# Kernel tuning notes

Measured on AMD Instinct MI355X. Metric: run time of the kernel, lower is better.

Reference implementation:

```python
import jax, jax.numpy as jnp
import numpy as np

D_MODEL = 1024
N_HEADS = 16
HEAD_DIM = D_MODEL // N_HEADS
D_FF = 4096
EPS = 1e-5


def setup_inputs() -> dict:
    key = jax.random.key(0)
    ks = jax.random.split(key, 12)
    s = 0.02
    return {
        "x": jax.random.normal(ks[0], (2, 2048, D_MODEL), jnp.float32),
        "wq": jax.random.normal(ks[1], (D_MODEL, D_MODEL), jnp.float32) * s,
        "bq": jnp.zeros((D_MODEL,), jnp.float32),
        "wk": jax.random.normal(ks[2], (D_MODEL, D_MODEL), jnp.float32) * s,
        "bk": jnp.zeros((D_MODEL,), jnp.float32),
        "wv": jax.random.normal(ks[3], (D_MODEL, D_MODEL), jnp.float32) * s,
        "bv": jnp.zeros((D_MODEL,), jnp.float32),
        "wo": jax.random.normal(ks[4], (D_MODEL, D_MODEL), jnp.float32) * s,
        "bo": jnp.zeros((D_MODEL,), jnp.float32),
        "w1": jax.random.normal(ks[5], (D_MODEL, D_FF), jnp.float32) * s,
        "b1": jnp.zeros((D_FF,), jnp.float32),
        "w2": jax.random.normal(ks[6], (D_FF, D_MODEL), jnp.float32) * s,
        "b2": jnp.zeros((D_MODEL,), jnp.float32),
        "g1": jnp.ones((D_MODEL,), jnp.float32),
        "be1": jnp.zeros((D_MODEL,), jnp.float32),
        "g2": jnp.ones((D_MODEL,), jnp.float32),
        "be2": jnp.zeros((D_MODEL,), jnp.float32),
    }


def _layer_norm(x, g, b):
    mu = jnp.mean(x, axis=-1, keepdims=True)
    var = jnp.var(x, axis=-1, keepdims=True)
    return (x - mu) * jax.lax.rsqrt(var + EPS) * g + b


def reference(x, wq, bq, wk, bk, wv, bv, wo, bo, w1, b1, w2, b2, g1, be1, g2, be2):
    B, S, D = x.shape
    nx = _layer_norm(x, g1, be1)
    # projections -> [B, H, S, d]
    def split_heads(t):
        return t.reshape(B, S, N_HEADS, HEAD_DIM).transpose(0, 2, 1, 3)
    q = split_heads(nx @ wq + bq)
    k = split_heads(nx @ wk + bk)
    v = split_heads(nx @ wv + bv)
    scores = jnp.einsum("bhqd,bhkd->bhqk", q, k) / jnp.sqrt(jnp.float32(HEAD_DIM))
    attn = jax.nn.softmax(scores, axis=-1)
    out = jnp.einsum("bhqk,bhkd->bhqd", attn, v)
    out = out.transpose(0, 2, 1, 3).reshape(B, S, D)
    x = x + (out @ wo + bo)
    nx = _layer_norm(x, g2, be2)
    ff = jax.nn.relu(nx @ w1 + b1) @ w2 + b2
    return x + ff
```

## Files before the change

### kernel.cpp

```cpp
#include <hip/hip_runtime.h>


typedef __attribute__((ext_vector_type(8))) unsigned short u16x8;
typedef __attribute__((ext_vector_type(4))) unsigned short u16x4;
typedef __attribute__((ext_vector_type(8))) __bf16 bf16x8;
typedef __attribute__((ext_vector_type(4))) float f32x4;
typedef __attribute__((ext_vector_type(4))) unsigned int u32x4;

#define C_SCALE 0.1803368801111f

static __device__ __forceinline__ unsigned short f2b(float f) {
    return __builtin_bit_cast(unsigned short, (__bf16)f);
}
static __device__ __forceinline__ float b2f(unsigned short h) {
    unsigned u = ((unsigned)h) << 16;
    float f;
    __builtin_memcpy(&f, &u, 4);
    return f;
}

static __device__ __forceinline__ void async_cp16(
    const unsigned short* g, unsigned short* l)
{
    __builtin_amdgcn_global_load_lds(
        (const __attribute__((address_space(1))) unsigned int*)g,
        (__attribute__((address_space(3))) unsigned int*)l,
        16, 0, 0);
}

__global__ __launch_bounds__(256) void transpose_all_k(
    const float* __restrict__ wq, const float* __restrict__ wk,
    const float* __restrict__ wv, const float* __restrict__ wo,
    const float* __restrict__ w1, const float* __restrict__ w2,
    unsigned short* __restrict__ wqkvT, unsigned short* __restrict__ woT,
    unsigned short* __restrict__ w1T, unsigned short* __restrict__ w2T)
{
    __shared__ unsigned short tile[32][33];
    const int ti = blockIdx.x;
    const float* in;
    unsigned short* out;
    int R, C, bi, bj;
    float sc = 1.0f;
    if (ti < 4096) {
        R = 1024; C = 1024;
        bi = (ti & 1023) >> 5; bj = ti & 31;
        int z = ti >> 10;
        in = (z == 0) ? wq : (z == 1) ? wk : (z == 2) ? wv : wo;
        out = (z < 3) ? wqkvT + (size_t)z * 1024 * 1024 : woT;
        if (z == 1) sc = C_SCALE;
    } else if (ti < 8192) {
        R = 1024; C = 4096;
        int l = ti - 4096;
        bi = l >> 7; bj = l & 127;
        in = w1; out = w1T;
    } else {
        R = 4096; C = 1024;
        int l = ti - 8192;
        bi = l >> 5; bj = l & 31;
        in = w2; out = w2T;
    }
    const int tx = threadIdx.x & 31, ty = threadIdx.x >> 5;
#pragma unroll
    for (int rr = 0; rr < 4; ++rr) {
        int r = ty + rr * 8;
        tile[r][tx] = f2b(in[(size_t)(bi * 32 + r) * C + bj * 32 + tx] * sc);
    }
    __syncthreads();
#pragma unroll
    for (int rr = 0; rr < 4; ++rr) {
        int r = ty + rr * 8;
        out[(size_t)(bj * 32 + r) * R + bi * 32 + tx] = tile[tx][r];
    }
}

__global__ __launch_bounds__(256) void concat3_k(
    const float* __restrict__ a, const float* __restrict__ b,
    const float* __restrict__ c, float* __restrict__ o)
{
    int t = blockIdx.x * 256 + threadIdx.x;
    float v = (t < 1024) ? a[t]
            : ((t < 2048) ? b[t - 1024] * C_SCALE : c[t - 2048]);
    o[t] = v;
}

__global__ __launch_bounds__(256) void ln_kernel(
    const float* __restrict__ x, const float* __restrict__ g,
    const float* __restrict__ be, unsigned short* __restrict__ o)
{
    const int row = blockIdx.x;
    const int t = threadIdx.x;
    const float* xr = x + (size_t)row * 1024;
    float4 v4 = *reinterpret_cast<const float4*>(&xr[t * 4]);
    float f[4] = {v4.x, v4.y, v4.z, v4.w};
    float s = f[0] + f[1] + f[2] + f[3];
    float ss = f[0] * f[0] + f[1] * f[1] + f[2] * f[2] + f[3] * f[3];
#pragma unroll
    for (int d = 1; d < 64; d <<= 1) {
        s += __shfl_xor(s, d);
        ss += __shfl_xor(ss, d);
    }
    __shared__ float sb[4], ssb[4];
    const int wave = t >> 6;
    if ((t & 63) == 0) { sb[wave] = s; ssb[wave] = ss; }
    __syncthreads();
    s = sb[0] + sb[1] + sb[2] + sb[3];
    ss = ssb[0] + ssb[1] + ssb[2] + ssb[3];
    const float mu = s * (1.0f / 1024.0f);
    const float var = ss * (1.0f / 1024.0f) - mu * mu;
    const float rs = rsqrtf(var + 1e-5f);
    u16x4 r4;
#pragma unroll
    for (int j = 0; j < 4; ++j)
        r4[j] = f2b((f[j] - mu) * rs * g[t * 4 + j] + be[t * 4 + j]);
    *reinterpret_cast<u16x4*>(&o[(size_t)row * 1024 + t * 4]) = r4;
}

__global__ __launch_bounds__(256) void reduce_ln_kernel(
    const unsigned short* __restrict__ pa, const unsigned short* __restrict__ pb,
    const float* __restrict__ bias, const float* __restrict__ x,
    const float* __restrict__ g, const float* __restrict__ be,
    float* __restrict__ x2, unsigned short* __restrict__ o)
{
    const int row = blockIdx.x;
    const int t = threadIdx.x;
    const size_t base = (size_t)row * 1024 + t * 4;
    float4 x4 = *reinterpret_cast<const float4*>(&x[base]);
    float4 bb = *reinterpret_cast<const float4*>(&bias[t * 4]);
    float f[4] = {x4.x + bb.x, x4.y + bb.y, x4.z + bb.z, x4.w + bb.w};
#pragma unroll
    for (int z = 0; z < 2; ++z) {
        u16x4 va = *reinterpret_cast<const u16x4*>(&pa[(size_t)z * 4096 * 1024 + base]);
        u16x4 vb = *reinterpret_cast<const u16x4*>(&pb[(size_t)z * 4096 * 1024 + base]);
#pragma unroll
        for (int j = 0; j < 4; ++j) f[j] += b2f(va[j]) + b2f(vb[j]);
    }
    *reinterpret_cast<float4*>(&x2[base]) = {f[0], f[1], f[2], f[3]};
    float s = f[0] + f[1] + f[2] + f[3];
    float ss = f[0] * f[0] + f[1] * f[1] + f[2] * f[2] + f[3] * f[3];
#pragma unroll
    for (int d = 1; d < 64; d <<= 1) {
        s += __shfl_xor(s, d);
        ss += __shfl_xor(ss, d);
    }
    __shared__ float sb[4], ssb[4];
    const int wave = t >> 6;
    if ((t & 63) == 0) { sb[wave] = s; ssb[wave] = ss; }
    __syncthreads();
    s = sb[0] + sb[1] + sb[2] + sb[3];
    ss = ssb[0] + ssb[1] + ssb[2] + ssb[3];
    const float mu = s * (1.0f / 1024.0f);
    const float var = ss * (1.0f / 1024.0f) - mu * mu;
    const float rs = rsqrtf(var + 1e-5f);
    u16x4 r4;
#pragma unroll
    for (int j = 0; j < 4; ++j)
        r4[j] = f2b((f[j] - mu) * rs * g[t * 4 + j] + be[t * 4 + j]);
    *reinterpret_cast<u16x4*>(&o[base]) = r4;
}

__global__ __launch_bounds__(256) void reduce_out4_k(
    const unsigned short* __restrict__ pa, const unsigned short* __restrict__ pb,
    const float* __restrict__ bias, const float* __restrict__ x2,
    float* __restrict__ out)
{
    const size_t i4 = ((size_t)blockIdx.x * 256 + threadIdx.x) * 4;
    float4 x4 = *reinterpret_cast<const float4*>(&x2[i4]);
    float4 bb = *reinterpret_cast<const float4*>(&bias[i4 & 1023]);
    float a0 = x4.x + bb.x, a1 = x4.y + bb.y, a2 = x4.z + bb.z, a3 = x4.w + bb.w;
#pragma unroll
    for (int z = 0; z < 2; ++z) {
        u16x4 va = *reinterpret_cast<const u16x4*>(&pa[(size_t)z * 4096 * 1024 + i4]);
        u16x4 vb = *reinterpret_cast<const u16x4*>(&pb[(size_t)z * 4096 * 1024 + i4]);
        a0 += b2f(va[0]) + b2f(vb[0]);
        a1 += b2f(va[1]) + b2f(vb[1]);
        a2 += b2f(va[2]) + b2f(vb[2]);
        a3 += b2f(va[3]) + b2f(vb[3]);
    }
    *reinterpret_cast<float4*>(&out[i4]) = {a0, a1, a2, a3};
}

template<int MODE, int RELU>
__global__ __launch_bounds__(512, 1) void gemm256(
    const unsigned short* __restrict__ A, int lda,
    const unsigned short* __restrict__ Bt, int ldb,
    const float* __restrict__ bias,
    void* __restrict__ Cv, void* __restrict__ Cv2, int N, int Kloop)
{
    __shared__ unsigned short lds[3 * 16384];
    const int t = threadIdx.x;
    const int wave = t >> 6, lane = t & 63;
    const int quad = lane >> 4, l16 = lane & 15;
    const int wm = wave >> 2, wn = wave & 3;
    const int m0 = blockIdx.y * 256;
    const int n0 = blockIdx.x * 256;
    const int k0 = blockIdx.z * Kloop;
    const int NT = Kloop >> 5;

    const int sc_row = t >> 2;
    const int sc_cb  = (t & 3) ^ ((t >> 3) & 3);
    const unsigned short* Asrc = &A[(size_t)(m0 + sc_row) * lda + k0 + sc_cb * 8];
    const unsigned short* Bsrc = &Bt[(size_t)(n0 + sc_row) * ldb + k0 + sc_cb * 8];
    const size_t Astep = (size_t)128 * lda;
    const size_t Bstep = (size_t)128 * ldb;
    unsigned short* dstA = &lds[t * 8];
    unsigned short* dstB = &lds[8192 + t * 8];

    const int cb = quad ^ ((l16 >> 1) & 3);
    const int aoff = (wm * 128 + l16) * 32 + cb * 8;
    const int boff = 8192 + (wn * 64 + l16) * 32 + cb * 8;

    f32x4 acc[8][4];
#pragma unroll
    for (int mi = 0; mi < 8; ++mi)
#pragma unroll
        for (int ni = 0; ni < 4; ++ni) acc[mi][ni] = {0.f, 0.f, 0.f, 0.f};

    async_cp16(Asrc, dstA);
    async_cp16(Asrc + Astep, dstA + 4096);
    async_cp16(Bsrc, dstB);
    async_cp16(Bsrc + Bstep, dstB + 4096);
    if (NT > 1) {
        async_cp16(Asrc + 32, dstA + 16384);
        async_cp16(Asrc + Astep + 32, dstA + 16384 + 4096);
        async_cp16(Bsrc + 32, dstB + 16384);
        async_cp16(Bsrc + Bstep + 32, dstB + 16384 + 4096);
        asm volatile("s_waitcnt vmcnt(4)\n\ts_barrier" ::: "memory");
    } else {
        asm volatile("s_waitcnt vmcnt(0)\n\ts_barrier" ::: "memory");
    }

    for (int tt = 0; tt < NT; ++tt) {
        const int b = tt - (tt / 3) * 3;
        const unsigned short* Lb = &lds[b * 16384];
        const int pf = tt + 2;
        const int bp = (pf < NT) ? (pf - (pf / 3) * 3) * 16384 : 0;
        bf16x8 af[8], bfr[4];
        if (pf < NT) {
            async_cp16(Asrc + (size_t)pf * 32, &lds[bp] + t * 8);
            async_cp16(Asrc + Astep + (size_t)pf * 32, &lds[bp] + t * 8 + 4096);
        }
#pragma unroll
        for (int mi = 0; mi < 8; ++mi)
            af[mi] = __builtin_bit_cast(bf16x8,
                *reinterpret_cast<const u16x8*>(&Lb[aoff + mi * 512]));
        bfr[0] = __builtin_bit_cast(bf16x8,
            *reinterpret_cast<const u16x8*>(&Lb[boff]));
        bfr[1] = __builtin_bit_cast(bf16x8,
            *reinterpret_cast<const u16x8*>(&Lb[boff + 512]));
        __builtin_amdgcn_s_setprio(1);
#pragma unroll
        for (int mi = 0; mi < 8; ++mi) {
            acc[mi][0] = __builtin_amdgcn_mfma_f32_16x16x32_bf16(
                af[mi], bfr[0], acc[mi][0], 0, 0, 0);
            acc[mi][1] = __builtin_amdgcn_mfma_f32_16x16x32_bf16(
                af[mi], bfr[1], acc[mi][1], 0, 0, 0);
        }
        __builtin_amdgcn_s_setprio(0);
        if (pf < NT) {
            async_cp16(Bsrc + (size_t)pf * 32, &lds[bp + 8192] + t * 8);
            async_cp16(Bsrc + Bstep + (size_t)pf * 32, &lds[bp + 8192] + t * 8 + 4096);
        }
        bfr[2] = __builtin_bit_cast(bf16x8,
            *reinterpret_cast<const u16x8*>(&Lb[boff + 1024]));
        bfr[3] = __builtin_bit_cast(bf16x8,
            *reinterpret_cast<const u16x8*>(&Lb[boff + 1536]));
        __builtin_amdgcn_s_setprio(1);
#pragma unroll
        for (int mi = 0; mi < 8; ++mi) {
            acc[mi][2] = __builtin_amdgcn_mfma_f32_16x16x32_bf16(
                af[mi], bfr[2], acc[mi][2], 0, 0, 0);
            acc[mi][3] = __builtin_amdgcn_mfma_f32_16x16x32_bf16(
                af[mi], bfr[3], acc[mi][3], 0, 0, 0);
        }
        __builtin_amdgcn_s_setprio(0);
        if (tt + 1 < NT) {
            if (pf < NT)
                asm volatile("s_waitcnt vmcnt(4)\n\ts_barrier" ::: "memory");
            else
                asm volatile("s_waitcnt vmcnt(0)\n\ts_barrier" ::: "memory");
        }
    }

#pragma unroll
    for (int mi = 0; mi < 8; ++mi) {
        const int gr0 = m0 + wm * 128 + mi * 16 + quad * 4;
#pragma unroll
        for (int ni = 0; ni < 4; ++ni) {
            const int gc = n0 + wn * 64 + ni * 16 + l16;
            if (MODE == 2) {
                const float bv = bias[gc];
                if (gc < 2048) {
#pragma unroll
                    for (int r = 0; r < 4; ++r)
                        ((unsigned short*)Cv)[(size_t)(gr0 + r) * 2048 + gc] =
                            f2b(acc[mi][ni][r] + bv);
                } else {
                    u16x4 pk;
#pragma unroll
                    for (int r = 0; r < 4; ++r) pk[r] = f2b(acc[mi][ni][r] + bv);
                    const int bb = gr0 >> 11, s0 = gr0 & 2047;
                    *reinterpret_cast<u16x4*>(
                        &((unsigned short*)Cv2)[((size_t)bb * 1024 + (gc - 2048)) * 2048 + s0]) = pk;
                }
            } else if (MODE == 5) {
                unsigned short* base = (blockIdx.z < 2)
                    ? (unsigned short*)Cv  + (size_t)blockIdx.z * 4096 * N
                    : (unsigned short*)Cv2 + (size_t)(blockIdx.z - 2) * 4096 * N;
#pragma unroll
                for (int r = 0; r < 4; ++r)
                    base[(size_t)(gr0 + r) * N + gc] = f2b(acc[mi][ni][r]);
            } else {
                const float bv = bias[gc];
#pragma unroll
                for (int r = 0; r < 4; ++r) {
                    float v = acc[mi][ni][r] + bv;
                    if (RELU) v = fmaxf(v, 0.f);
                    ((unsigned short*)Cv)[(size_t)(gr0 + r) * N + gc] = f2b(v);
                }
            }
        }
    }
}

__global__ __launch_bounds__(256, 2) void attn_kernel(
    const unsigned short* __restrict__ qkb, const unsigned short* __restrict__ vbT,
    unsigned short* __restrict__ ao)
{
    __shared__ unsigned short lds[3 * 8192];
    const int t = threadIdx.x;
    const int lane = t & 63;
    const int quad = lane >> 4, l16 = lane & 15;
    const int wave = t >> 6;
    const int bh = blockIdx.y;
    const int b = bh >> 4, h = bh & 15;
    const int q0 = blockIdx.x * 128 + wave * 32;
    const size_t qk_base = (size_t)b * 2048 * 2048;
    const size_t vt_base = (size_t)b * 1024 * 2048 + (size_t)h * 64 * 2048;

    bf16x8 qf[2][2];
#pragma unroll
    for (int m = 0; m < 2; ++m)
#pragma unroll
        for (int kk = 0; kk < 2; ++kk)
            qf[m][kk] = __builtin_bit_cast(bf16x8, *reinterpret_cast<const u16x8*>(
                &qkb[qk_base + (size_t)(q0 + m * 16 + l16) * 2048 + h * 64 + kk * 32 + quad * 8]));

    u16x8 ones_u;
#pragma unroll
    for (int j = 0; j < 8; ++j) ones_u[j] = 0x3F80;
    const bf16x8 onesf = __builtin_bit_cast(bf16x8, ones_u);

    f32x4 o_acc[2][4], l_frag[2];
#pragma unroll
    for (int m = 0; m < 2; ++m) {
        l_frag[m] = {0.f, 0.f, 0.f, 0.f};
#pragma unroll
        for (int nf = 0; nf < 4; ++nf) o_acc[m][nf] = {0.f, 0.f, 0.f, 0.f};
    }

    const int c0 = t, c1 = t + 256;
    const int r0 = c0 >> 3, r1 = c1 >> 3;
    const int scb0 = (c0 & 7) ^ (r0 & 7), scb1 = (c1 & 7) ^ (r1 & 7);
    const unsigned short* kS0 = &qkb[qk_base + (size_t)r0 * 2048 + 1024 + h * 64 + scb0 * 8];
    const unsigned short* kS1 = &qkb[qk_base + (size_t)r1 * 2048 + 1024 + h * 64 + scb1 * 8];
    const unsigned short* vS0 = &vbT[vt_base + (size_t)r0 * 2048 + scb0 * 8];
    const unsigned short* vS1 = &vbT[vt_base + (size_t)r1 * 2048 + scb1 * 8];

    const int off0 = l16 * 64 + ((quad ^ (l16 & 7)) * 8);

#define STAGE(tile, buf)                                                      \
    {                                                                         \
        const size_t ko = (size_t)(tile) * 64 * 2048;                         \
        const int vo = (tile) * 64;                                           \
        async_cp16(kS0 + ko, &lds[(buf) * 8192 + c0 * 8]);                    \
        async_cp16(kS1 + ko, &lds[(buf) * 8192 + c1 * 8]);                    \
        async_cp16(vS0 + vo, &lds[(buf) * 8192 + 4096 + c0 * 8]);             \
        async_cp16(vS1 + vo, &lds[(buf) * 8192 + 4096 + c1 * 8]);             \
    }

    STAGE(0, 0);
    STAGE(1, 1);
    asm volatile("s_waitcnt vmcnt(4)\n\ts_barrier" ::: "memory");

    for (int tt = 0; tt < 32; ++tt) {
        const int buf = tt - (tt / 3) * 3;
        const int pf = tt + 2;
        if (pf < 32) {
            const int bp = pf - (pf / 3) * 3;
            STAGE(pf, bp);
        }
        const unsigned short* LK = &lds[buf * 8192];
        const unsigned short* LV = LK + 4096;

        unsigned d0[2][4], d1[2][4];
#pragma unroll
        for (int kf = 0; kf < 4; ++kf) {
            bf16x8 kfr0 = __builtin_bit_cast(bf16x8,
                *reinterpret_cast<const u16x8*>(&LK[off0 + kf * 1024]));
            bf16x8 kfr1 = __builtin_bit_cast(bf16x8,
                *reinterpret_cast<const u16x8*>(&LK[(off0 ^ 32) + kf * 1024]));
#pragma unroll
            for (int m = 0; m < 2; ++m) {
                f32x4 s = {0.f, 0.f, 0.f, 0.f};
                s = __builtin_amdgcn_mfma_f32_16x16x32_bf16(kfr0, qf[m][0], s, 0, 0, 0);
                s = __builtin_amdgcn_mfma_f32_16x16x32_bf16(kfr1, qf[m][1], s, 0, 0, 0);
                d0[m][kf] = (unsigned)f2b(exp2f(s[0])) |
                            ((unsigned)f2b(exp2f(s[1])) << 16);
                d1[m][kf] = (unsigned)f2b(exp2f(s[2])) |
                            ((unsigned)f2b(exp2f(s[3])) << 16);
            }
        }
#pragma unroll
        for (int kh = 0; kh < 2; ++kh) {
            bf16x8 pfr[2];
#pragma unroll
            for (int m = 0; m < 2; ++m) {
                unsigned x0 = d0[m][kh * 2], y0 = d0[m][kh * 2 + 1];
                unsigned x1 = d1[m][kh * 2], y1 = d1[m][kh * 2 + 1];
                asm("v_permlane32_swap_b32 %0, %1\n\t"
                    "v_permlane16_swap_b32 %0, %1"
                    : "+v"(x0), "+v"(y0));
                asm("v_permlane32_swap_b32 %0, %1\n\t"
                    "v_permlane16_swap_b32 %0, %1"
                    : "+v"(x1), "+v"(y1));
                u32x4 pw = {x0, x1, y0, y1};
                pfr[m] = __builtin_bit_cast(bf16x8, pw);
                l_frag[m] = __builtin_amdgcn_mfma_f32_16x16x32_bf16(
                    pfr[m], onesf, l_frag[m], 0, 0, 0);
            }
            __builtin_amdgcn_s_setprio(1);
#pragma unroll
            for (int nf = 0; nf < 4; ++nf) {
                bf16x8 vfr = __builtin_bit_cast(bf16x8,
                    *reinterpret_cast<const u16x8*>(&LV[(off0 ^ (kh * 32)) + nf * 1024]));
#pragma unroll
                for (int m = 0; m < 2; ++m)
                    o_acc[m][nf] = __builtin_amdgcn_mfma_f32_16x16x32_bf16(
                        pfr[m], vfr, o_acc[m][nf], 0, 0, 0);
            }
            __builtin_amdgcn_s_setprio(0);
        }
        if (tt + 1 < 32) {
            if (pf < 32)
                asm volatile("s_waitcnt vmcnt(4)\n\ts_barrier" ::: "memory");
            else
                asm volatile("s_waitcnt vmcnt(0)\n\ts_barrier" ::: "memory");
        }
    }
#undef STAGE

#pragma unroll
    for (int m = 0; m < 2; ++m) {
#pragma unroll
        for (int r = 0; r < 4; ++r) {
            const float inv = 1.0f / l_frag[m][r];
            const int row = q0 + m * 16 + quad * 4 + r;
#pragma unroll
            for (int nf = 0; nf < 4; ++nf)
                ao[(size_t)b * 2048 * 1024 + (size_t)row * 1024 + h * 64 + nf * 16 + l16] =
                    f2b(o_acc[m][nf][r] * inv);
        }
    }
}

extern "C" void kernel_launch(void* const* d_in, const int* in_sizes, int n_in,
                              void* d_out, int out_size, void* d_ws, size_t ws_size,
                              hipStream_t stream)
{
    const float* x   = (const float*)d_in[0];
    const float* wq  = (const float*)d_in[1];
    const float* bq  = (const float*)d_in[2];
    const float* wk  = (const float*)d_in[3];
    const float* bk  = (const float*)d_in[4];
    const float* wv  = (const float*)d_in[5];
    const float* bv  = (const float*)d_in[6];
    const float* wo  = (const float*)d_in[7];
    const float* bo  = (const float*)d_in[8];
    const float* w1  = (const float*)d_in[9];
    const float* b1  = (const float*)d_in[10];
    const float* w2  = (const float*)d_in[11];
    const float* b2  = (const float*)d_in[12];
    const float* g1  = (const float*)d_in[13];
    const float* be1 = (const float*)d_in[14];
    const float* g2  = (const float*)d_in[15];
    const float* be2 = (const float*)d_in[16];
    float* out = (float*)d_out;
    char*  ws  = (char*)d_ws;

    const int M = 4096, D = 1024, DFF = 4096;
    const size_t MB = 1 << 20;

    unsigned short* wqkvT = (unsigned short*)(ws + 0 * MB);
    unsigned short* woT   = (unsigned short*)(ws + 6 * MB);
    unsigned short* w1T   = (unsigned short*)(ws + 8 * MB);
    unsigned short* w2T   = (unsigned short*)(ws + 16 * MB);
    unsigned short* ln    = (unsigned short*)(ws + 24 * MB);
    unsigned short* qkb   = (unsigned short*)(ws + 32 * MB);
    unsigned short* vbT   = (unsigned short*)(ws + 48 * MB);
    unsigned short* ao    = (unsigned short*)(ws + 56 * MB);
    unsigned short* ff1   = (unsigned short*)(ws + 32 * MB);
    float*          x2    = (float*)(ws + 64 * MB);
    float*          bqkv  = (float*)(ws + 80 * MB);
    unsigned short* pHi   = (unsigned short*)(ws + 80 * MB);
    unsigned short* pOlo  = (unsigned short*)(ws + 32 * MB);
    unsigned short* pFlo  = (unsigned short*)(ws + 0 * MB);

    transpose_all_k<<<12288, 256, 0, stream>>>(wq, wk, wv, wo, w1, w2,
                                               wqkvT, woT, w1T, w2T);
    concat3_k<<<12, 256, 0, stream>>>(bq, bk, bv, bqkv);
    ln_kernel<<<M, 256, 0, stream>>>(x, g1, be1, ln);
    gemm256<2, 0><<<dim3(12, 16), 512, 0, stream>>>(
        ln, D, wqkvT, D, bqkv, qkb, vbT, 3072, D);
    attn_kernel<<<dim3(16, 32), 256, 0, stream>>>(qkb, vbT, ao);
    gemm256<5, 0><<<dim3(4, 16, 4), 512, 0, stream>>>(
        ao, D, woT, D, nullptr, pHi, pOlo, 1024, 256);
    reduce_ln_kernel<<<M, 256, 0, stream>>>(pHi, pOlo, bo, x, g2, be2, x2, ln);
    gemm256<0, 1><<<dim3(16, 16), 512, 0, stream>>>(
        ln, D, w1T, D, b1, ff1, nullptr, DFF, D);
    gemm256<5, 0><<<dim3(4, 16, 4), 512, 0, stream>>>(
        ff1, DFF, w2T, DFF, nullptr, pHi, pFlo, 1024, 1024);
    reduce_out4_k<<<4096, 256, 0, stream>>>(pHi, pFlo, b2, x2, out);
}
```

Baseline: 354.1 us.

## Switch GEMM to double-buffered BK=64 stages with 8-chunk XOR swizzle

The 256x256 GEMM kernel moves from a triple-buffered pipeline with 32-wide K slices to a double-buffered pipeline with 64-wide K slices, using 128 KB of LDS. The LDS layout and XOR swizzle change to 8 chunks per row, and each iteration runs two 32-wide MFMA half-steps. The aim is to halve the number of barriers and loop iterations and to issue larger batches of async copies. The cost is a shallower prefetch, since each step now waits for vmcnt(0) rather than keeping a stage in flight, which can expose global memory latency.

```diff
diff --git a/kernel.cpp b/kernel.cpp
--- a/kernel.cpp
+++ b/kernel.cpp
@@ -186,7 +186,7 @@
     const float* __restrict__ bias,
     void* __restrict__ Cv, void* __restrict__ Cv2, int N, int Kloop)
 {
-    __shared__ unsigned short lds[3 * 16384];
+    __shared__ unsigned short lds[65536];
     const int t = threadIdx.x;
     const int wave = t >> 6, lane = t & 63;
     const int quad = lane >> 4, l16 = lane & 15;
@@ -194,20 +194,35 @@
     const int m0 = blockIdx.y * 256;
     const int n0 = blockIdx.x * 256;
     const int k0 = blockIdx.z * Kloop;
-    const int NT = Kloop >> 5;
-
-    const int sc_row = t >> 2;
-    const int sc_cb  = (t & 3) ^ ((t >> 3) & 3);
-    const unsigned short* Asrc = &A[(size_t)(m0 + sc_row) * lda + k0 + sc_cb * 8];
-    const unsigned short* Bsrc = &Bt[(size_t)(n0 + sc_row) * ldb + k0 + sc_cb * 8];
-    const size_t Astep = (size_t)128 * lda;
-    const size_t Bstep = (size_t)128 * ldb;
-    unsigned short* dstA = &lds[t * 8];
-    unsigned short* dstB = &lds[8192 + t * 8];
-
-    const int cb = quad ^ ((l16 >> 1) & 3);
-    const int aoff = (wm * 128 + l16) * 32 + cb * 8;
-    const int boff = 8192 + (wn * 64 + l16) * 32 + cb * 8;
+    const int NT = Kloop >> 6;
+
+    const unsigned short* Ap[4];
+    const unsigned short* Bp[4];
+#pragma unroll
+    for (int j = 0; j < 4; ++j) {
+        const int c = t + j * 512;
+        const int row = c >> 3;
+        const int gcb = (c & 7) ^ (row & 7);
+        Ap[j] = &A[(size_t)(m0 + row) * lda + k0 + gcb * 8];
+        Bp[j] = &Bt[(size_t)(n0 + row) * ldb + k0 + gcb * 8];
+    }
+    auto GSTAGE = [&](int buf) {
+        unsigned short* La = &lds[buf * 32768];
+        unsigned short* LbB = La + 16384;
+#pragma unroll
+        for (int j = 0; j < 4; ++j) {
+            async_cp16(Ap[j], &La[(t + j * 512) * 8]);
+            async_cp16(Bp[j], &LbB[(t + j * 512) * 8]);
+            Ap[j] += 64;
+            Bp[j] += 64;
+        }
+    };
+
+    const int swz = l16 & 7;
+    const int arow = (wm * 128 + l16) * 64;
+    const int brow = 16384 + (wn * 64 + l16) * 64;
+    const int cb0 = (quad ^ swz) * 8;
+    const int cb1 = ((4 + quad) ^ swz) * 8;
 
     f32x4 acc[8][4];
 #pragma unroll
@@ -215,70 +230,47 @@
 #pragma unroll
         for (int ni = 0; ni < 4; ++ni) acc[mi][ni] = {0.f, 0.f, 0.f, 0.f};
 
-    async_cp16(Asrc, dstA);
-    async_cp16(Asrc + Astep, dstA + 4096);
-    async_cp16(Bsrc, dstB);
-    async_cp16(Bsrc + Bstep, dstB + 4096);
-    if (NT > 1) {
-        async_cp16(Asrc + 32, dstA + 16384);
-        async_cp16(Asrc + Astep + 32, dstA + 16384 + 4096);
-        async_cp16(Bsrc + 32, dstB + 16384);
-        async_cp16(Bsrc + Bstep + 32, dstB + 16384 + 4096);
-        asm volatile("s_waitcnt vmcnt(4)\n\ts_barrier" ::: "memory");
-    } else {
-        asm volatile("s_waitcnt vmcnt(0)\n\ts_barrier" ::: "memory");
-    }
+    GSTAGE(0);
+    asm volatile("s_waitcnt vmcnt(0)\n\ts_barrier" ::: "memory");
 
     for (int tt = 0; tt < NT; ++tt) {
-        const int b = tt - (tt / 3) * 3;
-        const unsigned short* Lb = &lds[b * 16384];
-        const int pf = tt + 2;
-        const int bp = (pf < NT) ? (pf - (pf / 3) * 3) * 16384 : 0;
+        const unsigned short* Lb = &lds[(tt & 1) * 32768];
+        if (tt + 1 < NT) GSTAGE((tt + 1) & 1);
         bf16x8 af[8], bfr[4];
-        if (pf < NT) {
-            async_cp16(Asrc + (size_t)pf * 32, &lds[bp] + t * 8);
-            async_cp16(Asrc + Astep + (size_t)pf * 32, &lds[bp] + t * 8 + 4096);
-        }
 #pragma unroll
         for (int mi = 0; mi < 8; ++mi)
             af[mi] = __builtin_bit_cast(bf16x8,
-                *reinterpret_cast<const u16x8*>(&Lb[aoff + mi * 512]));
-        bfr[0] = __builtin_bit_cast(bf16x8,
-            *reinterpret_cast<const u16x8*>(&Lb[boff]));
-        bfr[1] = __builtin_bit_cast(bf16x8,
-            *reinterpret_cast<const u16x8*>(&Lb[boff + 512]));
+                *reinterpret_cast<const u16x8*>(&Lb[arow + mi * 1024 + cb0]));
+#pragma unroll
+        for (int ni = 0; ni < 4; ++ni)
+            bfr[ni] = __builtin_bit_cast(bf16x8,
+                *reinterpret_cast<const u16x8*>(&Lb[brow + ni * 1024 + cb0]));
         __builtin_amdgcn_s_setprio(1);
 #pragma unroll
-        for (int mi = 0; mi < 8; ++mi) {
-            acc[mi][0] = __builtin_amdgcn_mfma_f32_16x16x32_bf16(
-                af[mi], bfr[0], acc[mi][0], 0, 0, 0);
-            acc[mi][1] = __builtin_amdgcn_mfma_f32_16x16x32_bf16(
-                af[mi], bfr[1], acc[mi][1], 0, 0, 0);
-        }
+        for (int mi = 0; mi < 8; ++mi)
+#pragma unroll
+            for (int ni = 0; ni < 4; ++ni)
+                acc[mi][ni] = __builtin_amdgcn_mfma_f32_16x16x32_bf16(
+                    af[mi], bfr[ni], acc[mi][ni], 0, 0, 0);
         __builtin_amdgcn_s_setprio(0);
-        if (pf < NT) {
-            async_cp16(Bsrc + (size_t)pf * 32, &lds[bp + 8192] + t * 8);
-            async_cp16(Bsrc + Bstep + (size_t)pf * 32, &lds[bp + 8192] + t * 8 + 4096);
-        }
-        bfr[2] = __builtin_bit_cast(bf16x8,
-            *reinterpret_cast<const u16x8*>(&Lb[boff + 1024]));
-        bfr[3] = __builtin_bit_cast(bf16x8,
-            *reinterpret_cast<const u16x8*>(&Lb[boff + 1536]));
+#pragma unroll
+        for (int mi = 0; mi < 8; ++mi)
+            af[mi] = __builtin_bit_cast(bf16x8,
+                *reinterpret_cast<const u16x8*>(&Lb[arow + mi * 1024 + cb1]));
+#pragma unroll
+        for (int ni = 0; ni < 4; ++ni)
+            bfr[ni] = __builtin_bit_cast(bf16x8,
+                *reinterpret_cast<const u16x8*>(&Lb[brow + ni * 1024 + cb1]));
         __builtin_amdgcn_s_setprio(1);
 #pragma unroll
-        for (int mi = 0; mi < 8; ++mi) {
-            acc[mi][2] = __builtin_amdgcn_mfma_f32_16x16x32_bf16(
-                af[mi], bfr[2], acc[mi][2], 0, 0, 0);
-            acc[mi][3] = __builtin_amdgcn_mfma_f32_16x16x32_bf16(
-                af[mi], bfr[3], acc[mi][3], 0, 0, 0);
-        }
+        for (int mi = 0; mi < 8; ++mi)
+#pragma unroll
+            for (int ni = 0; ni < 4; ++ni)
+                acc[mi][ni] = __builtin_amdgcn_mfma_f32_16x16x32_bf16(
+                    af[mi], bfr[ni], acc[mi][ni], 0, 0, 0);
         __builtin_amdgcn_s_setprio(0);
-        if (tt + 1 < NT) {
-            if (pf < NT)
-                asm volatile("s_waitcnt vmcnt(4)\n\ts_barrier" ::: "memory");
-            else
-                asm volatile("s_waitcnt vmcnt(0)\n\ts_barrier" ::: "memory");
-        }
+        if (tt + 1 < NT)
+            asm volatile("s_waitcnt vmcnt(0)\n\ts_barrier" ::: "memory");
     }
 
 #pragma unroll
```

Result: no change. 358.1 us (+1.1%).

## Replace split-K 256-tile GEMMs with full-K 128-tile GEMM for N=1024 projections

Applied to the files above, without the earlier changes.

The output projection and the FFN down-projection previously used a 256x256 tile GEMM with 4-way split-K. That wrote four bf16 partial buffers, which the following reduction kernels had to sum. They now use a new 128x128 tile kernel with 256 threads and 2 blocks per CU, running over the full K with a single output, so the reductions read only one partial. This removes the extra partial-buffer traffic and the bf16 rounding of each partial, but each block now runs a longer serial K loop with smaller tiles and less operand reuse.

```diff
diff --git a/kernel.cpp b/kernel.cpp
--- a/kernel.cpp
+++ b/kernel.cpp
@@ -115,8 +115,8 @@
     *reinterpret_cast<u16x4*>(&o[(size_t)row * 1024 + t * 4]) = r4;
 }
 
-__global__ __launch_bounds__(256) void reduce_ln_kernel(
-    const unsigned short* __restrict__ pa, const unsigned short* __restrict__ pb,
+__global__ __launch_bounds__(256) void reduce1_ln_kernel(
+    const unsigned short* __restrict__ p,
     const float* __restrict__ bias, const float* __restrict__ x,
     const float* __restrict__ g, const float* __restrict__ be,
     float* __restrict__ x2, unsigned short* __restrict__ o)
@@ -126,14 +126,9 @@
     const size_t base = (size_t)row * 1024 + t * 4;
     float4 x4 = *reinterpret_cast<const float4*>(&x[base]);
     float4 bb = *reinterpret_cast<const float4*>(&bias[t * 4]);
-    float f[4] = {x4.x + bb.x, x4.y + bb.y, x4.z + bb.z, x4.w + bb.w};
-#pragma unroll
-    for (int z = 0; z < 2; ++z) {
-        u16x4 va = *reinterpret_cast<const u16x4*>(&pa[(size_t)z * 4096 * 1024 + base]);
-        u16x4 vb = *reinterpret_cast<const u16x4*>(&pb[(size_t)z * 4096 * 1024 + base]);
-#pragma unroll
-        for (int j = 0; j < 4; ++j) f[j] += b2f(va[j]) + b2f(vb[j]);
-    }
+    u16x4 vp = *reinterpret_cast<const u16x4*>(&p[base]);
+    float f[4] = {x4.x + bb.x + b2f(vp[0]), x4.y + bb.y + b2f(vp[1]),
+                  x4.z + bb.z + b2f(vp[2]), x4.w + bb.w + b2f(vp[3])};
     *reinterpret_cast<float4*>(&x2[base]) = {f[0], f[1], f[2], f[3]};
     float s = f[0] + f[1] + f[2] + f[3];
     float ss = f[0] * f[0] + f[1] * f[1] + f[2] * f[2] + f[3] * f[3];
@@ -158,25 +153,18 @@
     *reinterpret_cast<u16x4*>(&o[base]) = r4;
 }
 
-__global__ __launch_bounds__(256) void reduce_out4_k(
-    const unsigned short* __restrict__ pa, const unsigned short* __restrict__ pb,
+__global__ __launch_bounds__(256) void reduce1_out_k(
+    const unsigned short* __restrict__ p,
     const float* __restrict__ bias, const float* __restrict__ x2,
     float* __restrict__ out)
 {
     const size_t i4 = ((size_t)blockIdx.x * 256 + threadIdx.x) * 4;
     float4 x4 = *reinterpret_cast<const float4*>(&x2[i4]);
     float4 bb = *reinterpret_cast<const float4*>(&bias[i4 & 1023]);
-    float a0 = x4.x + bb.x, a1 = x4.y + bb.y, a2 = x4.z + bb.z, a3 = x4.w + bb.w;
-#pragma unroll
-    for (int z = 0; z < 2; ++z) {
-        u16x4 va = *reinterpret_cast<const u16x4*>(&pa[(size_t)z * 4096 * 1024 + i4]);
-        u16x4 vb = *reinterpret_cast<const u16x4*>(&pb[(size_t)z * 4096 * 1024 + i4]);
-        a0 += b2f(va[0]) + b2f(vb[0]);
-        a1 += b2f(va[1]) + b2f(vb[1]);
-        a2 += b2f(va[2]) + b2f(vb[2]);
-        a3 += b2f(va[3]) + b2f(vb[3]);
-    }
-    *reinterpret_cast<float4*>(&out[i4]) = {a0, a1, a2, a3};
+    u16x4 vp = *reinterpret_cast<const u16x4*>(&p[i4]);
+    *reinterpret_cast<float4*>(&out[i4]) = {
+        x4.x + bb.x + b2f(vp[0]), x4.y + bb.y + b2f(vp[1]),
+        x4.z + bb.z + b2f(vp[2]), x4.w + bb.w + b2f(vp[3])};
 }
 
 template<int MODE, int RELU>
@@ -302,13 +290,6 @@
                     *reinterpret_cast<u16x4*>(
                         &((unsigned short*)Cv2)[((size_t)bb * 1024 + (gc - 2048)) * 2048 + s0]) = pk;
                 }
-            } else if (MODE == 5) {
-                unsigned short* base = (blockIdx.z < 2)
-                    ? (unsigned short*)Cv  + (size_t)blockIdx.z * 4096 * N
-                    : (unsigned short*)Cv2 + (size_t)(blockIdx.z - 2) * 4096 * N;
-#pragma unroll
-                for (int r = 0; r < 4; ++r)
-                    base[(size_t)(gr0 + r) * N + gc] = f2b(acc[mi][ni][r]);
             } else {
                 const float bv = bias[gc];
 #pragma unroll
@@ -317,6 +298,102 @@
                     if (RELU) v = fmaxf(v, 0.f);
                     ((unsigned short*)Cv)[(size_t)(gr0 + r) * N + gc] = f2b(v);
                 }
+            }
+        }
+    }
+}
+
+template<int RELU>
+__global__ __launch_bounds__(256, 2) void gemm128(
+    const unsigned short* __restrict__ A, int lda,
+    const unsigned short* __restrict__ Bt, int ldb,
+    unsigned short* __restrict__ C, int N, int K)
+{
+    __shared__ unsigned short lds[3 * 8192];
+    const int t = threadIdx.x;
+    const int wave = t >> 6, lane = t & 63;
+    const int quad = lane >> 4, l16 = lane & 15;
+    const int wm = wave >> 1, wn = wave & 1;
+    const int m0 = blockIdx.y * 128;
+    const int n0 = blockIdx.x * 128;
+    const int NT = K >> 5;
+
+    const int c0 = t, c1 = t + 256;
+    const int r0 = c0 >> 2, r1 = c1 >> 2;
+    const int sb0 = (c0 & 3) ^ (r0 & 3), sb1 = (c1 & 3) ^ (r1 & 3);
+    const unsigned short* Aq0 = &A[(size_t)(m0 + r0) * lda + sb0 * 8];
+    const unsigned short* Aq1 = &A[(size_t)(m0 + r1) * lda + sb1 * 8];
+    const unsigned short* Bq0 = &Bt[(size_t)(n0 + r0) * ldb + sb0 * 8];
+    const unsigned short* Bq1 = &Bt[(size_t)(n0 + r1) * ldb + sb1 * 8];
+
+    const int scb = (quad ^ (l16 & 3)) * 8;
+    const int aoff = (wm * 64 + l16) * 32 + scb;
+    const int boff = 4096 + (wn * 64 + l16) * 32 + scb;
+
+    f32x4 acc[4][4];
+#pragma unroll
+    for (int mi = 0; mi < 4; ++mi)
+#pragma unroll
+        for (int ni = 0; ni < 4; ++ni) acc[mi][ni] = {0.f, 0.f, 0.f, 0.f};
+
+#define STAGE128(tile, buf)                                                   \
+    {                                                                         \
+        const int ko = (tile) * 32;                                           \
+        async_cp16(Aq0 + ko, &lds[(buf) * 8192 + c0 * 8]);                    \
+        async_cp16(Aq1 + ko, &lds[(buf) * 8192 + c1 * 8]);                    \
+        async_cp16(Bq0 + ko, &lds[(buf) * 8192 + 4096 + c0 * 8]);             \
+        async_cp16(Bq1 + ko, &lds[(buf) * 8192 + 4096 + c1 * 8]);             \
+    }
+
+    STAGE128(0, 0);
+    STAGE128(1, 1);
+    asm volatile("s_waitcnt vmcnt(4)\n\ts_barrier" ::: "memory");
+
+    for (int tt = 0; tt < NT; ++tt) {
+        const int buf = tt - (tt / 3) * 3;
+        const int pf = tt + 2;
+        if (pf < NT) {
+            const int bp = pf - (pf / 3) * 3;
+            STAGE128(pf, bp);
+        }
+        const unsigned short* Lb = &lds[buf * 8192];
+        bf16x8 af[4], bfr[4];
+#pragma unroll
+        for (int mi = 0; mi < 4; ++mi)
+            af[mi] = __builtin_bit_cast(bf16x8,
+                *reinterpret_cast<const u16x8*>(&Lb[aoff + mi * 512]));
+#pragma unroll
+        for (int ni = 0; ni < 4; ++ni)
+            bfr[ni] = __builtin_bit_cast(bf16x8,
+                *reinterpret_cast<const u16x8*>(&Lb[boff + ni * 512]));
+        __builtin_amdgcn_s_setprio(1);
+#pragma unroll
+        for (int mi = 0; mi < 4; ++mi)
+#pragma unroll
+            for (int ni = 0; ni < 4; ++ni)
+                acc[mi][ni] = __builtin_amdgcn_mfma_f32_16x16x32_bf16(
+                    af[mi], bfr[ni], acc[mi][ni], 0, 0, 0);
+        __builtin_amdgcn_s_setprio(0);
+        if (tt + 1 < NT) {
+            if (pf < NT)
+                asm volatile("s_waitcnt vmcnt(4)\n\ts_barrier" ::: "memory");
+            else
+                asm volatile("s_waitcnt vmcnt(0)\n\ts_barrier" ::: "memory");
+        }
+    }
+#undef STAGE128
+
+#pragma unroll
+    for (int mi = 0; mi < 4; ++mi) {
+        const int gr0 = m0 + wm * 64 + mi * 16 + quad * 4;
+#pragma unroll
+        for (int ni = 0; ni < 4; ++ni) {
+            const int gc = n0 + wn * 64 + ni * 16 + l16;
+#pragma unroll
+            for (int r = 0; r < 4; ++r) {
+                float v = acc[mi][ni][r];
+                if (RELU) v = fmaxf(v, 0.f);
+                C[(size_t)(gr0 + r) * N + gc] = f2b(v);
             }
         }
     }
@@ -501,9 +578,7 @@
     unsigned short* ff1   = (unsigned short*)(ws + 32 * MB);
     float*          x2    = (float*)(ws + 64 * MB);
     float*          bqkv  = (float*)(ws + 80 * MB);
-    unsigned short* pHi   = (unsigned short*)(ws + 80 * MB);
-    unsigned short* pOlo  = (unsigned short*)(ws + 32 * MB);
-    unsigned short* pFlo  = (unsigned short*)(ws + 0 * MB);
+    unsigned short* P1    = (unsigned short*)(ws + 88 * MB);
 
     transpose_all_k<<<12288, 256, 0, stream>>>(wq, wk, wv, wo, w1, w2,
                                                wqkvT, woT, w1T, w2T);
@@ -512,12 +587,10 @@
     gemm256<2, 0><<<dim3(12, 16), 512, 0, stream>>>(
         ln, D, wqkvT, D, bqkv, qkb, vbT, 3072, D);
     attn_kernel<<<dim3(16, 32), 256, 0, stream>>>(qkb, vbT, ao);
-    gemm256<5, 0><<<dim3(4, 16, 4), 512, 0, stream>>>(
-        ao, D, woT, D, nullptr, pHi, pOlo, 1024, 256);
-    reduce_ln_kernel<<<M, 256, 0, stream>>>(pHi, pOlo, bo, x, g2, be2, x2, ln);
+    gemm128<0><<<dim3(8, 32), 256, 0, stream>>>(ao, D, woT, D, P1, 1024, D);
+    reduce1_ln_kernel<<<M, 256, 0, stream>>>(P1, bo, x, g2, be2, x2, ln);
     gemm256<0, 1><<<dim3(16, 16), 512, 0, stream>>>(
         ln, D, w1T, D, b1, ff1, nullptr, DFF, D);
-    gemm256<5, 0><<<dim3(4, 16, 4), 512, 0, stream>>>(
-        ff1, DFF, w2T, DFF, nullptr, pHi, pFlo, 1024, 1024);
-    reduce_out4_k<<<4096, 256, 0, stream>>>(pHi, pFlo, b2, x2, out);
-}
+    gemm128<0><<<dim3(8, 32), 256, 0, stream>>>(ff1, DFF, w2T, DFF, P1, 1024, DFF);
+    reduce1_out_k<<<4096, 256, 0, stream>>>(P1, b2, x2, out);
+}
```

New measurement: 362.4 us. 1.02x slower.
